# Kernel optimization log

Measured on AMD Instinct MI355X. Metric: run time of the kernel, lower is better.

The kernel has to match this reference:

```python
import jax, jax.numpy as jnp
import numpy as np

HEAD_DIM = 128

def setup_inputs() -> dict:
    key = jax.random.key(0)
    k1, k2, k3 = jax.random.split(key, 3)
    B, S, H, Hkv, D = 2, 2048, 32, 8, HEAD_DIM
    q = jax.random.normal(k1, (B, S, H, D), dtype=jnp.float32)
    k = jax.random.normal(k2, (B, S, Hkv, D), dtype=jnp.float32)
    v = jax.random.normal(k3, (B, S, Hkv, D), dtype=jnp.float32)
    return {"q": q, "k": k, "v": v}

def reference(q, k, v):
    # Causal GQA attention, same math as SDPA(is_causal=True, scale=head_dim**-0.5)
    # q: [B,S,H,D], k/v: [B,S,Hkv,D]; H = Hkv * G (grouped-query attention)
    B, S, H, D = q.shape
    Hkv = k.shape[2]
    G = H // Hkv
    scale = jnp.asarray(D, q.dtype) ** -0.5
    qg = q.reshape(B, S, Hkv, G, D)
    # scores: [B, Hkv, G, Sq, Sk]
    scores = jnp.einsum('bqhgd,bkhd->bhgqk', qg, k) * scale
    causal = jnp.tril(jnp.ones((S, S), dtype=bool))  # [Sq, Sk]
    scores = jnp.where(causal, scores, jnp.asarray(-jnp.inf, scores.dtype))
    probs = jax.nn.softmax(scores, axis=-1)
    out = jnp.einsum('bhgqk,bkhd->bqhgd', probs, v)
    return out.reshape(B, S, H, D)
```

## Files before the change

### kernel.cpp

```cpp
#include <hip/hip_runtime.h>
#include <hip/hip_bf16.h>

typedef short bf16x8 __attribute__((ext_vector_type(8)));
typedef float f32x4  __attribute__((ext_vector_type(4)));

#define B_    2
#define S_    2048
#define H_    32
#define HKV_  8
#define D_    128
#define QBLK  64
#define QBLK2 128
#define KVB   32
#define SCALE 0.1275431741f

static __device__ inline float exp2_fast(float x) {
    return __builtin_amdgcn_exp2f(x);
}

static __device__ inline unsigned short f2bf(float f) {
    unsigned u = __builtin_bit_cast(unsigned, f);
    u += 0x7fffu + ((u >> 16) & 1u);
    return (unsigned short)(u >> 16);
}
static __device__ inline unsigned pk2(float a, float b) {
    return (unsigned)f2bf(a) | ((unsigned)f2bf(b) << 16);
}
static __device__ inline short cvt_bf(float f) {
    __hip_bfloat16 h = __float2bfloat16(f);
    return __builtin_bit_cast(short, h);
}
static __device__ inline void gload16(const unsigned char* g, unsigned char* l) {
    __builtin_amdgcn_global_load_lds(
        (const __attribute__((address_space(1))) void*)g,
        (__attribute__((address_space(3))) void*)l, 16, 0, 0);
}

__global__ __launch_bounds__(256) void prep_k(const float* __restrict__ Kg,
                                              unsigned char* __restrict__ Kb) {
    const int s   = blockIdx.x * 256 + threadIdx.x;
    const int seg = s & 15;
    const int kv  = (s >> 4) & (S_ - 1);
    const int bhk = s >> 15;
    const int hk  = bhk & (HKV_ - 1);
    const int b   = bhk >> 3;
    const float* src = Kg + ((size_t)(b * S_ + kv) * HKV_ + hk) * D_ + seg * 8;
    float4 x0 = *(const float4*)(src);
    float4 x1 = *(const float4*)(src + 4);
    uint4 u = { pk2(x0.x, x0.y), pk2(x0.z, x0.w), pk2(x1.x, x1.y), pk2(x1.z, x1.w) };
    *(uint4*)(Kb + ((size_t)(b * HKV_ + hk) * S_ + kv) * 256 + ((seg * 16) ^ ((kv & 7) << 4))) = u;
}

__global__ __launch_bounds__(256) void prep_v(const float* __restrict__ Vg,
                                              unsigned short* __restrict__ Vb) {
    const int blk  = blockIdx.x;
    const int half = blk & 1;
    const int tile = (blk >> 1) & 63;
    const int hk   = (blk >> 7) & (HKV_ - 1);
    const int b    = blk >> 10;
    const int t    = threadIdx.x;
    const int kp0  = (t & 3) * 8;
    const int d    = (t >> 2) + half * 64;
    const int kv0  = tile * KVB;
    unsigned short tmp[8];
#pragma unroll
    for (int j = 0; j < 8; ++j) {
        const int kp = kp0 + j;
        const int kv = (((kp >> 2) & 1) << 4) + ((kp >> 3) << 2) + (kp & 3);
        tmp[j] = f2bf(Vg[((size_t)(b * S_ + kv0 + kv) * HKV_ + hk) * D_ + d]);
    }
    unsigned short* dst = Vb + ((size_t)(b * HKV_ + hk) * 64 + tile) * (128 * 32) + d * 32 + kp0;
    *(uint4*)dst = *(uint4*)tmp;
}

__global__ __launch_bounds__(256) void fattn2(
        const float* __restrict__ Qg, const unsigned char* __restrict__ Kb,
        const unsigned char* __restrict__ Vb, float* __restrict__ Og) {
    __shared__ __align__(16) unsigned char lds[2 * 16384];

    const int tid  = threadIdx.x;
    const int lane = tid & 63;
    const int w    = tid >> 6;
    const int m    = lane & 15;
    const int g    = lane >> 4;
    const int lane16 = lane * 16;

    const int SQ  = S_ / QBLK2;
    const int bid = blockIdx.x;
    const int qt  = (SQ - 1) - (bid >> 6);
    const int hb  = bid & 63;
    const int h   = hb & (H_ - 1);
    const int b   = hb >> 5;
    const int hk  = h >> 2;

    const int qB    = qt * QBLK2;
    const int q0w   = qB + w * 32;
    const int qA    = q0w + m;
    const int qgate = q0w + 31;

    const unsigned char* KbH = Kb + (size_t)(b * HKV_ + hk) * S_ * 256;
    const unsigned char* VbH = Vb + (size_t)(b * HKV_ + hk) * 64 * 8192;

    bf16x8 qfA[4], qfB[4];
    {
        const float* qrowA = Qg + (size_t)((b * S_ + qA) * H_ + h) * D_;
        const float* qrowB = qrowA + (size_t)16 * H_ * D_;
#pragma unroll
        for (int db = 0; db < 4; ++db) {
            const float* pA = qrowA + db * 32 + g * 8;
            const float* pB = qrowB + db * 32 + g * 8;
            float4 a0 = *(const float4*)(pA);
            float4 a1 = *(const float4*)(pA + 4);
            float4 b0 = *(const float4*)(pB);
            float4 b1 = *(const float4*)(pB + 4);
            bf16x8 qa, qb;
            qa[0] = cvt_bf(a0.x * SCALE); qa[1] = cvt_bf(a0.y * SCALE);
            qa[2] = cvt_bf(a0.z * SCALE); qa[3] = cvt_bf(a0.w * SCALE);
            qa[4] = cvt_bf(a1.x * SCALE); qa[5] = cvt_bf(a1.y * SCALE);
            qa[6] = cvt_bf(a1.z * SCALE); qa[7] = cvt_bf(a1.w * SCALE);
            qb[0] = cvt_bf(b0.x * SCALE); qb[1] = cvt_bf(b0.y * SCALE);
            qb[2] = cvt_bf(b0.z * SCALE); qb[3] = cvt_bf(b0.w * SCALE);
            qb[4] = cvt_bf(b1.x * SCALE); qb[5] = cvt_bf(b1.y * SCALE);
            qb[6] = cvt_bf(b1.z * SCALE); qb[7] = cvt_bf(b1.w * SCALE);
            qfA[db] = qa; qfB[db] = qb;
        }
    }

    f32x4 oaccA[8], oaccB[8];
#pragma unroll
    for (int i = 0; i < 8; ++i) {
        oaccA[i] = (f32x4){0.f, 0.f, 0.f, 0.f};
        oaccB[i] = (f32x4){0.f, 0.f, 0.f, 0.f};
    }
    float m_run = 4.0f, lsumA = 0.f, lsumB = 0.f;

#define STAGE(kt, c) do {                                                     \
        const unsigned char* KbT = KbH + (size_t)(kt) * (KVB * 256);          \
        const unsigned char* VbT = VbH + (size_t)(kt) * 8192;                 \
        unsigned char* dK = lds + (c) * 16384;                                \
        unsigned char* dV = dK + 8192;                                        \
        gload16(KbT + (w * 2 + 0) * 1024 + lane16, dK + (w * 2 + 0) * 1024);  \
        gload16(KbT + (w * 2 + 1) * 1024 + lane16, dK + (w * 2 + 1) * 1024);  \
        gload16(VbT + (w * 2 + 0) * 1024 + lane16, dV + (w * 2 + 0) * 1024);  \
        gload16(VbT + (w * 2 + 1) * 1024 + lane16, dV + (w * 2 + 1) * 1024);  \
    } while (0)

    const int nt = (qB + QBLK2) / KVB;
    int cur = 0;
    STAGE(0, 0);

    for (int t = 0; t < nt; ++t) {
        const int kv0 = t * KVB;
        if (t + 1 < nt) {
            STAGE(t + 1, cur ^ 1);
            asm volatile("s_waitcnt vmcnt(4)" ::: "memory");
        } else {
            asm volatile("s_waitcnt vmcnt(0)" ::: "memory");
        }
        __builtin_amdgcn_s_barrier();

        if (kv0 <= qgate) {
            const unsigned char* cK = lds + cur * 16384;
            const unsigned char* cV = cK + 8192;

            f32x4 stA0 = (f32x4){0.f,0.f,0.f,0.f}, stA1 = stA0;
            f32x4 stB0 = stA0, stB1 = stA0;
            const int sw = (m & 7) << 4;
            __builtin_amdgcn_s_setprio(1);
#pragma unroll
            for (int db = 0; db < 4; ++db) {
                bf16x8 kf0 = *(const bf16x8*)(cK + (m     ) * 256 + ((db * 64 + g * 16) ^ sw));
                bf16x8 kf1 = *(const bf16x8*)(cK + (m + 16) * 256 + ((db * 64 + g * 16) ^ sw));
                stA0 = __builtin_amdgcn_mfma_f32_16x16x32_bf16(kf0, qfA[db], stA0, 0, 0, 0);
                stA1 = __builtin_amdgcn_mfma_f32_16x16x32_bf16(kf1, qfA[db], stA1, 0, 0, 0);
                stB0 = __builtin_amdgcn_mfma_f32_16x16x32_bf16(kf0, qfB[db], stB0, 0, 0, 0);
                stB1 = __builtin_amdgcn_mfma_f32_16x16x32_bf16(kf1, qfB[db], stB1, 0, 0, 0);
            }
            __builtin_amdgcn_s_setprio(0);

            float pA[8], pB[8];
#pragma unroll
            for (int jj = 0; jj < 4; ++jj) {
                pA[jj] = stA0[jj]; pA[4 + jj] = stA1[jj];
                pB[jj] = stB0[jj]; pB[4 + jj] = stB1[jj];
            }
            if (kv0 + (KVB - 1) > q0w) {
                const int qBrow = qA + 16;
#pragma unroll
                for (int jj = 0; jj < 4; ++jj) {
                    const int kva = kv0 + g * 4 + jj;
                    if (kva      > qA)    pA[jj]     = -1e30f;
                    if (kva + 16 > qA)    pA[4 + jj] = -1e30f;
                    if (kva      > qBrow) pB[jj]     = -1e30f;
                    if (kva + 16 > qBrow) pB[4 + jj] = -1e30f;
                }
            }

            float pmax = fmaxf(
                fmaxf(fmaxf(fmaxf(pA[0], pA[1]), fmaxf(pA[2], pA[3])),
                      fmaxf(fmaxf(pA[4], pA[5]), fmaxf(pA[6], pA[7]))),
                fmaxf(fmaxf(fmaxf(pB[0], pB[1]), fmaxf(pB[2], pB[3])),
                      fmaxf(fmaxf(pB[4], pB[5]), fmaxf(pB[6], pB[7]))));
            if (__any(pmax > m_run + 12.0f)) {
                float tm = fmaxf(pmax, __shfl_xor(pmax, 16));
                tm = fmaxf(tm, __shfl_xor(tm, 32));
                const float m_new = fmaxf(m_run, tm);
                const float corr  = exp2_fast(m_run - m_new);
                lsumA *= corr; lsumB *= corr;
                float cj[4];
#pragma unroll
                for (int jj = 0; jj < 4; ++jj) cj[jj] = __shfl(corr, g * 4 + jj);
#pragma unroll
                for (int i = 0; i < 8; ++i)
#pragma unroll
                    for (int jj = 0; jj < 4; ++jj) {
                        oaccA[i][jj] *= cj[jj];
                        oaccB[i][jj] *= cj[jj];
                    }
                m_run = m_new;
            }

#pragma unroll
            for (int i = 0; i < 8; ++i) pA[i] = exp2_fast(pA[i] - m_run);
#pragma unroll
            for (int i = 0; i < 8; ++i) pB[i] = exp2_fast(pB[i] - m_run);
            lsumA += ((pA[0] + pA[1]) + (pA[2] + pA[3])) + ((pA[4] + pA[5]) + (pA[6] + pA[7]));
            lsumB += ((pB[0] + pB[1]) + (pB[2] + pB[3])) + ((pB[4] + pB[5]) + (pB[6] + pB[7]));

            bf16x8 paA, paB;
#pragma unroll
            for (int i = 0; i < 8; ++i) { paA[i] = cvt_bf(pA[i]); paB[i] = cvt_bf(pB[i]); }

            __builtin_amdgcn_s_setprio(1);
#pragma unroll
            for (int db8 = 0; db8 < 8; ++db8) {
                bf16x8 vf = *(const bf16x8*)(cV + (db8 * 16 + m) * 64 + g * 16);
                oaccA[db8] = __builtin_amdgcn_mfma_f32_16x16x32_bf16(paA, vf, oaccA[db8], 0, 0, 0);
                oaccB[db8] = __builtin_amdgcn_mfma_f32_16x16x32_bf16(paB, vf, oaccB[db8], 0, 0, 0);
            }
            __builtin_amdgcn_s_setprio(0);
        }
        asm volatile("" ::: "memory");
        __builtin_amdgcn_s_barrier();
        cur ^= 1;
    }
#undef STAGE

    lsumA += __shfl_xor(lsumA, 16); lsumA += __shfl_xor(lsumA, 32);
    lsumB += __shfl_xor(lsumB, 16); lsumB += __shfl_xor(lsumB, 32);
    const float rA = 1.0f / lsumA, rB = 1.0f / lsumB;
    float rsA[4], rsB[4];
#pragma unroll
    for (int jj = 0; jj < 4; ++jj) {
        rsA[jj] = __shfl(rA, g * 4 + jj);
        rsB[jj] = __shfl(rB, g * 4 + jj);
    }
#pragma unroll
    for (int db8 = 0; db8 < 8; ++db8) {
#pragma unroll
        for (int jj = 0; jj < 4; ++jj) {
            const int qrA = q0w + g * 4 + jj;
            Og[(size_t)((b * S_ + qrA) * H_ + h) * D_ + db8 * 16 + m]
                = oaccA[db8][jj] * rsA[jj];
            Og[(size_t)((b * S_ + qrA + 16) * H_ + h) * D_ + db8 * 16 + m]
                = oaccB[db8][jj] * rsB[jj];
        }
    }
}

__global__ __launch_bounds__(256) void fattn_fallback(
        const float* __restrict__ Qg, const float* __restrict__ Kg,
        const float* __restrict__ Vg, float* __restrict__ Og) {
    __shared__ __align__(16) unsigned char  sK[32 * 256];
    __shared__ __align__(16) unsigned short sV[128 * 40];
    const int tid  = threadIdx.x;
    const int lane = tid & 63;
    const int w    = tid >> 6;
    const int m    = lane & 15;
    const int g    = lane >> 4;
    const int SQ = S_ / QBLK;
    const int bid = blockIdx.x;
    const int qt  = bid % SQ;
    const int h   = (bid / SQ) % H_;
    const int b   = bid / (SQ * H_);
    const int hk  = h >> 2;
    const int qB    = qt * QBLK;
    const int q0w   = qB + w * 16;
    const int q_abs = q0w + m;
    const float SC = 0.08838834764831845f;
    bf16x8 qf[4];
    {
        const float* qrow = Qg + (size_t)((b * S_ + q_abs) * H_ + h) * D_;
#pragma unroll
        for (int db = 0; db < 4; ++db) {
            const float* p = qrow + db * 32 + g * 8;
            float4 a = *(const float4*)(p);
            float4 c = *(const float4*)(p + 4);
            bf16x8 q8;
            q8[0] = (short)f2bf(a.x * SC); q8[1] = (short)f2bf(a.y * SC);
            q8[2] = (short)f2bf(a.z * SC); q8[3] = (short)f2bf(a.w * SC);
            q8[4] = (short)f2bf(c.x * SC); q8[5] = (short)f2bf(c.y * SC);
            q8[6] = (short)f2bf(c.z * SC); q8[7] = (short)f2bf(c.w * SC);
            qf[db] = q8;
        }
    }
    f32x4 oacc[8];
#pragma unroll
    for (int i = 0; i < 8; ++i) oacc[i] = (f32x4){0.f, 0.f, 0.f, 0.f};
    float m_run = -1e30f, lsum = 0.f;
    const int nt = (qB + QBLK) / KVB;
    for (int t = 0; t < nt; ++t) {
        const int kv0 = t * KVB;
        __syncthreads();
        {
            const int r = tid >> 3, seg = tid & 7;
            const float* src = Kg + (size_t)((b * S_ + kv0 + r) * HKV_ + hk) * D_ + seg * 16;
            float4 x0 = *(const float4*)(src + 0);
            float4 x1 = *(const float4*)(src + 4);
            float4 x2 = *(const float4*)(src + 8);
            float4 x3 = *(const float4*)(src + 12);
            uint4 u0 = { pk2(x0.x,x0.y), pk2(x0.z,x0.w), pk2(x1.x,x1.y), pk2(x1.z,x1.w) };
            uint4 u1 = { pk2(x2.x,x2.y), pk2(x2.z,x2.w), pk2(x3.x,x3.y), pk2(x3.z,x3.w) };
            const int colb = seg * 32;
            const int sw   = (r & 7) << 4;
            *(uint4*)(sK + r * 256 + ((colb     ) ^ sw)) = u0;
            *(uint4*)(sK + r * 256 + ((colb + 16) ^ sw)) = u1;
        }
        {
            const int kv = tid & 31, d0 = (tid >> 5) * 16;
            const int kp = (((kv & 15) >> 2) << 3) + ((kv >> 4) << 2) + (kv & 3);
            const float* src = Vg + (size_t)((b * S_ + kv0 + kv) * HKV_ + hk) * D_ + d0;
#pragma unroll
            for (int i = 0; i < 4; ++i) {
                float4 x = *(const float4*)(src + i * 4);
                const int d = d0 + i * 4;
                sV[(d + 0) * 40 + kp] = f2bf(x.x);
                sV[(d + 1) * 40 + kp] = f2bf(x.y);
                sV[(d + 2) * 40 + kp] = f2bf(x.z);
                sV[(d + 3) * 40 + kp] = f2bf(x.w);
            }
        }
        __syncthreads();
        if (kv0 > q0w + 15) continue;
        f32x4 st0 = (f32x4){0.f,0.f,0.f,0.f}, st1 = st0;
#pragma unroll
        for (int db = 0; db < 4; ++db) {
            const int sw = (m & 7) << 4;
            bf16x8 kf0 = *(const bf16x8*)(sK + (m      ) * 256 + ((db * 64 + g * 16) ^ sw));
            bf16x8 kf1 = *(const bf16x8*)(sK + (m + 16 ) * 256 + ((db * 64 + g * 16) ^ sw));
            st0 = __builtin_amdgcn_mfma_f32_16x16x32_bf16(kf0, qf[db], st0, 0, 0, 0);
            st1 = __builtin_amdgcn_mfma_f32_16x16x32_bf16(kf1, qf[db], st1, 0, 0, 0);
        }
        float p[8];
        float tm = -1e30f;
#pragma unroll
        for (int jj = 0; jj < 4; ++jj) {
            int kva = kv0 + g * 4 + jj;
            float s0 = (kva       <= q_abs) ? st0[jj] : -1e30f;
            float s1 = (kva + 16  <= q_abs) ? st1[jj] : -1e30f;
            p[jj]     = s0;
            p[4 + jj] = s1;
            tm = fmaxf(tm, fmaxf(s0, s1));
        }
        tm = fmaxf(tm, __shfl_xor(tm, 16));
        tm = fmaxf(tm, __shfl_xor(tm, 32));
        const float m_new = fmaxf(m_run, tm);
        const float corr  = __expf(m_run - m_new);
        float ls = 0.f;
#pragma unroll
        for (int i = 0; i < 8; ++i) { float e = __expf(p[i] - m_new); p[i] = e; ls += e; }
        ls += __shfl_xor(ls, 16);
        ls += __shfl_xor(ls, 32);
        lsum  = lsum * corr + ls;
        m_run = m_new;
        float cj[4];
#pragma unroll
        for (int jj = 0; jj < 4; ++jj) cj[jj] = __shfl(corr, g * 4 + jj);
#pragma unroll
        for (int i = 0; i < 8; ++i)
#pragma unroll
            for (int jj = 0; jj < 4; ++jj) oacc[i][jj] *= cj[jj];
        bf16x8 pa;
#pragma unroll
        for (int i = 0; i < 8; ++i) pa[i] = (short)f2bf(p[i]);
#pragma unroll
        for (int db8 = 0; db8 < 8; ++db8) {
            bf16x8 vf = *(const bf16x8*)((const unsigned char*)sV +
                          (((db8 * 16 + m) * 40 + g * 8) * 2));
            oacc[db8] = __builtin_amdgcn_mfma_f32_16x16x32_bf16(pa, vf, oacc[db8], 0, 0, 0);
        }
    }
    float rs[4];
    const float rinv = 1.0f / lsum;
#pragma unroll
    for (int jj = 0; jj < 4; ++jj) rs[jj] = __shfl(rinv, g * 4 + jj);
#pragma unroll
    for (int db8 = 0; db8 < 8; ++db8) {
#pragma unroll
        for (int jj = 0; jj < 4; ++jj) {
            const int qr = q0w + g * 4 + jj;
            Og[(size_t)((b * S_ + qr) * H_ + h) * D_ + db8 * 16 + m] = oacc[db8][jj] * rs[jj];
        }
    }
}

extern "C" void kernel_launch(void* const* d_in, const int* in_sizes, int n_in,
                              void* d_out, int out_size, void* d_ws, size_t ws_size,
                              hipStream_t stream) {
    const float* q = (const float*)d_in[0];
    const float* k = (const float*)d_in[1];
    const float* v = (const float*)d_in[2];
    float* o = (float*)d_out;

    const size_t KB_BYTES = (size_t)B_ * HKV_ * S_ * 256;
    const size_t VB_BYTES = (size_t)B_ * HKV_ * 64 * 128 * 32 * 2;

    if (ws_size >= KB_BYTES + VB_BYTES) {
        unsigned char*  Kb = (unsigned char*)d_ws;
        unsigned short* Vb = (unsigned short*)((unsigned char*)d_ws + KB_BYTES);
        prep_k<<<2048, 256, 0, stream>>>(k, Kb);
        prep_v<<<2048, 256, 0, stream>>>(v, Vb);
        const int blocks = B_ * H_ * (S_ / QBLK2);
        fattn2<<<blocks, 256, 0, stream>>>(q, Kb, (const unsigned char*)Vb, o);
    } else {
        const int blocks = B_ * H_ * (S_ / QBLK);
        fattn_fallback<<<blocks, 256, 0, stream>>>(q, k, v, o);
    }
}
```

Baseline: 123.0 us.

## Pair mirrored causal query tiles per block to balance work

Each block now takes two 64-row query tiles, tile j and its mirror 31-j, so every block has about the same causal KV length. The old scheme gave one 128-row tile per block, which made per-block work very uneven. The A-tile compute is skipped once KV passes its causal limit, and launch bounds now request 4 blocks per CU. In exchange, the shared K/V tiles are reused across fewer co-located rows in the early iterations, and the A-path branches add control overhead.

Measured after the change: 324.6 us. 2.64x slower.

```diff
diff --git a/kernel.cpp b/kernel.cpp
--- a/kernel.cpp
+++ b/kernel.cpp
@@ -10,7 +10,6 @@
 #define HKV_  8
 #define D_    128
 #define QBLK  64
-#define QBLK2 128
 #define KVB   32
 #define SCALE 0.1275431741f
 
@@ -73,7 +72,7 @@
     *(uint4*)dst = *(uint4*)tmp;
 }
 
-__global__ __launch_bounds__(256) void fattn2(
+__global__ __launch_bounds__(256, 4) void fattn3(
         const float* __restrict__ Qg, const unsigned char* __restrict__ Kb,
         const unsigned char* __restrict__ Vb, float* __restrict__ Og) {
     __shared__ __align__(16) unsigned char lds[2 * 16384];
@@ -85,26 +84,27 @@
     const int g    = lane >> 4;
     const int lane16 = lane * 16;
 
-    const int SQ  = S_ / QBLK2;
     const int bid = blockIdx.x;
-    const int qt  = (SQ - 1) - (bid >> 6);
+    const int j   = bid >> 6;
     const int hb  = bid & 63;
     const int h   = hb & (H_ - 1);
     const int b   = hb >> 5;
     const int hk  = h >> 2;
 
-    const int qB    = qt * QBLK2;
-    const int q0w   = qB + w * 32;
-    const int qA    = q0w + m;
-    const int qgate = q0w + 31;
+    const int qAb = j * 64 + w * 16;
+    const int qBb = (31 - j) * 64 + w * 16;
+    const int qAr = qAb + m;
+    const int qBr = qBb + m;
+    const int qgateA = qAb + 15;
+    const int qgateB = qBb + 15;
 
     const unsigned char* KbH = Kb + (size_t)(b * HKV_ + hk) * S_ * 256;
     const unsigned char* VbH = Vb + (size_t)(b * HKV_ + hk) * 64 * 8192;
 
     bf16x8 qfA[4], qfB[4];
     {
-        const float* qrowA = Qg + (size_t)((b * S_ + qA) * H_ + h) * D_;
-        const float* qrowB = qrowA + (size_t)16 * H_ * D_;
+        const float* qrowA = Qg + (size_t)((b * S_ + qAr) * H_ + h) * D_;
+        const float* qrowB = Qg + (size_t)((b * S_ + qBr) * H_ + h) * D_;
 #pragma unroll
         for (int db = 0; db < 4; ++db) {
             const float* pA = qrowA + db * 32 + g * 8;
@@ -145,7 +145,7 @@
         gload16(VbT + (w * 2 + 1) * 1024 + lane16, dV + (w * 2 + 1) * 1024);  \
     } while (0)
 
-    const int nt = (qB + QBLK2) / KVB;
+    const int nt = 2 * (32 - j);
     int cur = 0;
     STAGE(0, 0);
 
@@ -159,48 +159,64 @@
         }
         __builtin_amdgcn_s_barrier();
 
-        if (kv0 <= qgate) {
+        if (kv0 <= qgateB) {
             const unsigned char* cK = lds + cur * 16384;
             const unsigned char* cV = cK + 8192;
-
-            f32x4 stA0 = (f32x4){0.f,0.f,0.f,0.f}, stA1 = stA0;
-            f32x4 stB0 = stA0, stB1 = stA0;
             const int sw = (m & 7) << 4;
+            const bool actA = (kv0 <= qgateA);
+
+            f32x4 stB0 = (f32x4){0.f,0.f,0.f,0.f}, stB1 = stB0;
             __builtin_amdgcn_s_setprio(1);
 #pragma unroll
             for (int db = 0; db < 4; ++db) {
                 bf16x8 kf0 = *(const bf16x8*)(cK + (m     ) * 256 + ((db * 64 + g * 16) ^ sw));
                 bf16x8 kf1 = *(const bf16x8*)(cK + (m + 16) * 256 + ((db * 64 + g * 16) ^ sw));
-                stA0 = __builtin_amdgcn_mfma_f32_16x16x32_bf16(kf0, qfA[db], stA0, 0, 0, 0);
-                stA1 = __builtin_amdgcn_mfma_f32_16x16x32_bf16(kf1, qfA[db], stA1, 0, 0, 0);
                 stB0 = __builtin_amdgcn_mfma_f32_16x16x32_bf16(kf0, qfB[db], stB0, 0, 0, 0);
                 stB1 = __builtin_amdgcn_mfma_f32_16x16x32_bf16(kf1, qfB[db], stB1, 0, 0, 0);
             }
+            f32x4 stA0 = (f32x4){0.f,0.f,0.f,0.f}, stA1 = stA0;
+            if (actA) {
+#pragma unroll
+                for (int db = 0; db < 4; ++db) {
+                    bf16x8 kf0 = *(const bf16x8*)(cK + (m     ) * 256 + ((db * 64 + g * 16) ^ sw));
+                    bf16x8 kf1 = *(const bf16x8*)(cK + (m + 16) * 256 + ((db * 64 + g * 16) ^ sw));
+                    stA0 = __builtin_amdgcn_mfma_f32_16x16x32_bf16(kf0, qfA[db], stA0, 0, 0, 0);
+                    stA1 = __builtin_amdgcn_mfma_f32_16x16x32_bf16(kf1, qfA[db], stA1, 0, 0, 0);
+                }
+            }
             __builtin_amdgcn_s_setprio(0);
 
-            float pA[8], pB[8];
-#pragma unroll
-            for (int jj = 0; jj < 4; ++jj) {
-                pA[jj] = stA0[jj]; pA[4 + jj] = stA1[jj];
-                pB[jj] = stB0[jj]; pB[4 + jj] = stB1[jj];
-            }
-            if (kv0 + (KVB - 1) > q0w) {
-                const int qBrow = qA + 16;
+            float pB[8];
+#pragma unroll
+            for (int jj = 0; jj < 4; ++jj) { pB[jj] = stB0[jj]; pB[4 + jj] = stB1[jj]; }
+            if (kv0 + (KVB - 1) > qBb) {
 #pragma unroll
                 for (int jj = 0; jj < 4; ++jj) {
                     const int kva = kv0 + g * 4 + jj;
-                    if (kva      > qA)    pA[jj]     = -1e30f;
-                    if (kva + 16 > qA)    pA[4 + jj] = -1e30f;
-                    if (kva      > qBrow) pB[jj]     = -1e30f;
-                    if (kva + 16 > qBrow) pB[4 + jj] = -1e30f;
+                    if (kva      > qBr) pB[jj]     = -1e30f;
+                    if (kva + 16 > qBr) pB[4 + jj] = -1e30f;
                 }
             }
-
-            float pmax = fmaxf(
-                fmaxf(fmaxf(fmaxf(pA[0], pA[1]), fmaxf(pA[2], pA[3])),
-                      fmaxf(fmaxf(pA[4], pA[5]), fmaxf(pA[6], pA[7]))),
-                fmaxf(fmaxf(fmaxf(pB[0], pB[1]), fmaxf(pB[2], pB[3])),
-                      fmaxf(fmaxf(pB[4], pB[5]), fmaxf(pB[6], pB[7]))));
+            float pmax = fmaxf(fmaxf(fmaxf(pB[0], pB[1]), fmaxf(pB[2], pB[3])),
+                               fmaxf(fmaxf(pB[4], pB[5]), fmaxf(pB[6], pB[7])));
+
+            float pA[8];
+            if (actA) {
+#pragma unroll
+                for (int jj = 0; jj < 4; ++jj) { pA[jj] = stA0[jj]; pA[4 + jj] = stA1[jj]; }
+                if (kv0 + (KVB - 1) > qAb) {
+#pragma unroll
+                    for (int jj = 0; jj < 4; ++jj) {
+                        const int kva = kv0 + g * 4 + jj;
+                        if (kva      > qAr) pA[jj]     = -1e30f;
+                        if (kva + 16 > qAr) pA[4 + jj] = -1e30f;
+                    }
+                }
+                pmax = fmaxf(pmax,
+                       fmaxf(fmaxf(fmaxf(pA[0], pA[1]), fmaxf(pA[2], pA[3])),
+                             fmaxf(fmaxf(pA[4], pA[5]), fmaxf(pA[6], pA[7]))));
+            }
+
             if (__any(pmax > m_run + 12.0f)) {
                 float tm = fmaxf(pmax, __shfl_xor(pmax, 16));
                 tm = fmaxf(tm, __shfl_xor(tm, 32));
@@ -221,22 +237,33 @@
             }
 
 #pragma unroll
-            for (int i = 0; i < 8; ++i) pA[i] = exp2_fast(pA[i] - m_run);
-#pragma unroll
             for (int i = 0; i < 8; ++i) pB[i] = exp2_fast(pB[i] - m_run);
-            lsumA += ((pA[0] + pA[1]) + (pA[2] + pA[3])) + ((pA[4] + pA[5]) + (pA[6] + pA[7]));
             lsumB += ((pB[0] + pB[1]) + (pB[2] + pB[3])) + ((pB[4] + pB[5]) + (pB[6] + pB[7]));
-
-            bf16x8 paA, paB;
-#pragma unroll
-            for (int i = 0; i < 8; ++i) { paA[i] = cvt_bf(pA[i]); paB[i] = cvt_bf(pB[i]); }
+            bf16x8 paB;
+#pragma unroll
+            for (int i = 0; i < 8; ++i) paB[i] = cvt_bf(pB[i]);
+
+            bf16x8 paA;
+            if (actA) {
+#pragma unroll
+                for (int i = 0; i < 8; ++i) pA[i] = exp2_fast(pA[i] - m_run);
+                lsumA += ((pA[0] + pA[1]) + (pA[2] + pA[3])) + ((pA[4] + pA[5]) + (pA[6] + pA[7]));
+#pragma unroll
+                for (int i = 0; i < 8; ++i) paA[i] = cvt_bf(pA[i]);
+            }
 
             __builtin_amdgcn_s_setprio(1);
 #pragma unroll
             for (int db8 = 0; db8 < 8; ++db8) {
                 bf16x8 vf = *(const bf16x8*)(cV + (db8 * 16 + m) * 64 + g * 16);
-                oaccA[db8] = __builtin_amdgcn_mfma_f32_16x16x32_bf16(paA, vf, oaccA[db8], 0, 0, 0);
                 oaccB[db8] = __builtin_amdgcn_mfma_f32_16x16x32_bf16(paB, vf, oaccB[db8], 0, 0, 0);
+            }
+            if (actA) {
+#pragma unroll
+                for (int db8 = 0; db8 < 8; ++db8) {
+                    bf16x8 vf = *(const bf16x8*)(cV + (db8 * 16 + m) * 64 + g * 16);
+                    oaccA[db8] = __builtin_amdgcn_mfma_f32_16x16x32_bf16(paA, vf, oaccA[db8], 0, 0, 0);
+                }
             }
             __builtin_amdgcn_s_setprio(0);
         }
@@ -259,10 +286,11 @@
     for (int db8 = 0; db8 < 8; ++db8) {
 #pragma unroll
         for (int jj = 0; jj < 4; ++jj) {
-            const int qrA = q0w + g * 4 + jj;
+            const int qrA = qAb + g * 4 + jj;
+            const int qrB = qBb + g * 4 + jj;
             Og[(size_t)((b * S_ + qrA) * H_ + h) * D_ + db8 * 16 + m]
                 = oaccA[db8][jj] * rsA[jj];
-            Og[(size_t)((b * S_ + qrA + 16) * H_ + h) * D_ + db8 * 16 + m]
+            Og[(size_t)((b * S_ + qrB) * H_ + h) * D_ + db8 * 16 + m]
                 = oaccB[db8][jj] * rsB[jj];
         }
     }
@@ -420,8 +448,7 @@
         unsigned short* Vb = (unsigned short*)((unsigned char*)d_ws + KB_BYTES);
         prep_k<<<2048, 256, 0, stream>>>(k, Kb);
         prep_v<<<2048, 256, 0, stream>>>(v, Vb);
-        const int blocks = B_ * H_ * (S_ / QBLK2);
-        fattn2<<<blocks, 256, 0, stream>>>(q, Kb, (const unsigned char*)Vb, o);
+        fattn3<<<1024, 256, 0, stream>>>(q, Kb, (const unsigned char*)Vb, o);
     } else {
         const int blocks = B_ * H_ * (S_ / QBLK);
         fattn_fallback<<<blocks, 256, 0, stream>>>(q, k, v, o);
```
